# Optimization experiments

Measured on AMD Instinct MI355X. Metric: run time of the kernel, lower is better.

The kernel has to match this reference:

```python
import jax, jax.numpy as jnp
import numpy as np

EMBED_DIM = 768
NUM_HEADS = 12
FF_DIM = 3072
HEAD_DIM = EMBED_DIM // NUM_HEADS
LN_EPS = 1e-5


def setup_inputs() -> dict:
    key = jax.random.key(0)
    ks = jax.random.split(key, 10)
    C, F = EMBED_DIM, FF_DIM
    s = lambda d: 1.0 / np.sqrt(d)
    return {
        "x": jax.random.normal(ks[0], (2, 2048, C), dtype=jnp.float32),
        "w_qkv": jax.random.normal(ks[1], (C, 3 * C), dtype=jnp.float32) * s(C),
        "w_out": jax.random.normal(ks[2], (C, C), dtype=jnp.float32) * s(C),
        "ln1_g": jnp.ones((C,), jnp.float32),
        "ln1_b": jnp.zeros((C,), jnp.float32),
        "ln2_g": jnp.ones((C,), jnp.float32),
        "ln2_b": jnp.zeros((C,), jnp.float32),
        "w1": jax.random.normal(ks[3], (C, F), dtype=jnp.float32) * s(C),
        "b1": jnp.zeros((F,), jnp.float32),
        "w2": jax.random.normal(ks[4], (F, C), dtype=jnp.float32) * s(F),
        "b2": jnp.zeros((C,), jnp.float32),
    }


def _layernorm(x, g, b):
    mu = jnp.mean(x, axis=-1, keepdims=True)
    var = jnp.var(x, axis=-1, keepdims=True)
    return (x - mu) * jax.lax.rsqrt(var + LN_EPS) * g + b


def _attention(x, w_qkv, w_out):
    B, T, C = x.shape
    qkv = x @ w_qkv                               # [B,T,3C]
    q, k, v = jnp.split(qkv, 3, axis=2)
    def heads(t):  # [B,T,C] -> [B,H,T,Dh]
        return t.reshape(B, T, NUM_HEADS, HEAD_DIM).transpose(0, 2, 1, 3)
    q, k, v = heads(q), heads(k), heads(v)
    att = jnp.einsum("bhqd,bhkd->bhqk", q, k) / np.sqrt(HEAD_DIM)
    mask = jnp.tril(jnp.ones((T, T), bool))
    att = jnp.where(mask, att, -jnp.inf)
    att = jax.nn.softmax(att, axis=-1)
    out = jnp.einsum("bhqk,bhkd->bhqd", att, v)   # [B,H,T,Dh]
    out = out.transpose(0, 2, 1, 3).reshape(B, T, C)
    return out @ w_out


def reference(x, w_qkv, w_out, ln1_g, ln1_b, ln2_g, ln2_b, w1, b1, w2, b2):
    x = x + _attention(_layernorm(x, ln1_g, ln1_b), w_qkv, w_out)
    h = _layernorm(x, ln2_g, ln2_b)
    h = jax.nn.gelu(h @ w1 + b1, approximate=False) @ w2 + b2
    return x + h
```

## Files before the change

kernel.cpp:

```cpp
#include <hip/hip_runtime.h>
#include <hip/hip_bf16.h>
#include <math.h>

typedef __attribute__((ext_vector_type(8))) short short8;
typedef __attribute__((ext_vector_type(4))) float f32x4;
typedef __attribute__((address_space(1))) const void CG;
typedef __attribute__((address_space(3))) void LS;

#define LOAD_LDS16(src, dst) __builtin_amdgcn_global_load_lds((CG*)(src), (LS*)(dst), 16, 0, 0)

__device__ __forceinline__ short f2bf(float f) {
  union { float f; unsigned u; } v; v.f = f;
  unsigned r = v.u + 0x7fffu + ((v.u >> 16) & 1u);
  return (short)(r >> 16);
}

__global__ __launch_bounds__(256) void transp_all(const float* __restrict__ w_qkv,
                                                  const float* __restrict__ w_out,
                                                  const float* __restrict__ w1,
                                                  const float* __restrict__ w2,
                                                  short* __restrict__ wqkvT,
                                                  short* __restrict__ woutT,
                                                  short* __restrict__ w1T,
                                                  short* __restrict__ w2T) {
  __shared__ short t[32][33];
  int bid = blockIdx.x;
  const float* W; short* Wt; int K, N, nx, id;
  if (bid < 1728)      { W = w_qkv; Wt = wqkvT; K = 768;  N = 2304; nx = 72; id = bid; }
  else if (bid < 2304) { W = w_out; Wt = woutT; K = 768;  N = 768;  nx = 24; id = bid - 1728; }
  else if (bid < 4608) { W = w1;    Wt = w1T;   K = 768;  N = 3072; nx = 96; id = bid - 2304; }
  else                 { W = w2;    Wt = w2T;   K = 3072; N = 768;  nx = 24; id = bid - 4608; }
  int n0 = (id % nx) << 5, k0 = (id / nx) << 5;
  int tid = threadIdx.x;
#pragma unroll
  for (int p = 0; p < 4; ++p) {
    int e = tid + (p << 8);
    int r = e >> 5, c = e & 31;
    t[r][c] = f2bf(W[(size_t)(k0 + r) * N + n0 + c]);
  }
  __syncthreads();
#pragma unroll
  for (int p = 0; p < 4; ++p) {
    int e = tid + (p << 8);
    int r = e >> 5, c = e & 31;
    Wt[(size_t)(n0 + r) * K + k0 + c] = t[c][r];
  }
}

__global__ __launch_bounds__(256) void ln_kernel(const float* __restrict__ x,
                                                 const float* __restrict__ g,
                                                 const float* __restrict__ b,
                                                 short* __restrict__ out) {
  int row = blockIdx.x;
  const float* xr = x + (size_t)row * 768;
  int tid = threadIdx.x;
  float v0 = xr[tid], v1 = xr[tid + 256], v2 = xr[tid + 512];
  float s = v0 + v1 + v2;
  float ss = v0 * v0 + v1 * v1 + v2 * v2;
#pragma unroll
  for (int m = 1; m < 64; m <<= 1) { s += __shfl_xor(s, m); ss += __shfl_xor(ss, m); }
  __shared__ float red[8];
  int w = tid >> 6;
  if ((tid & 63) == 0) { red[w] = s; red[w + 4] = ss; }
  __syncthreads();
  s = red[0] + red[1] + red[2] + red[3];
  ss = red[4] + red[5] + red[6] + red[7];
  float mean = s * (1.0f / 768.0f);
  float var = ss * (1.0f / 768.0f) - mean * mean;
  float rs = rsqrtf(var + 1e-5f);
  short* outr = out + (size_t)row * 768;
  outr[tid]       = f2bf((v0 - mean) * rs * g[tid]       + b[tid]);
  outr[tid + 256] = f2bf((v1 - mean) * rs * g[tid + 256] + b[tid + 256]);
  outr[tid + 512] = f2bf((v2 - mean) * rs * g[tid + 512] + b[tid + 512]);
}

template <int EPI>
__global__ __launch_bounds__(256, 2) void gemm_bt(
    const short* __restrict__ A, const short* __restrict__ Bt,
    int M, int N, int K,
    short* __restrict__ outQ, short* __restrict__ outK, short* __restrict__ outVt,
    float* __restrict__ outF, short* __restrict__ outB,
    const float* __restrict__ bias, const float* __restrict__ resid) {
  __shared__ short lA[2][128 * 32];
  __shared__ short lB[2][128 * 32];
  int tid = threadIdx.x;
  int lane = tid & 63, w = tid >> 6;
  int li = lane & 15, g = lane >> 4;

  int nx = gridDim.x, ny = gridDim.y;
  int nwg = nx * ny;
  int fid = (int)blockIdx.y * nx + (int)blockIdx.x;
  int nid = (fid & 7) * (nwg >> 3) + (fid >> 3);
  const int GM = 8;
  int npg = GM * nx;
  int grp = nid / npg;
  int fm = grp * GM;
  int gs = min(GM, ny - fm);
  int lid = nid - grp * npg;
  int bm = (fm + lid % gs) << 7;
  int bn = (lid / gs) << 7;

  int wrow = (w >> 1) << 6, wcol = (w & 1) << 6;
  size_t lda = (EPI == 4) ? 3072 : (size_t)K;
  int koff = (EPI == 4) ? (int)blockIdx.z * 1536 : 0;

  const short* as[2];
  const short* bs[2];
#pragma unroll
  for (int p = 0; p < 2; ++p) {
    int v = tid + (p << 8);
    int row = v >> 2;
    int lc = (v & 3) ^ ((row ^ (row >> 2)) & 3);
    as[p] = A + (size_t)(bm + row) * lda + koff + lc * 8;
    bs[p] = Bt + (size_t)(bn + row) * lda + koff + lc * 8;
  }
  int sg = (g ^ ((li ^ (li >> 2)) & 3)) << 3;

  f32x4 zero = {0.f, 0.f, 0.f, 0.f};
  f32x4 acc[4][4];
#pragma unroll
  for (int i = 0; i < 4; ++i)
#pragma unroll
    for (int j = 0; j < 4; ++j) acc[i][j] = zero;

#define GSTAGE(buf, ki)                                                 \
  do {                                                                  \
    int kk = (ki) << 5;                                                 \
    LOAD_LDS16(as[0] + kk, (char*)lA[buf] + (w << 10));                 \
    LOAD_LDS16(as[1] + kk, (char*)lA[buf] + 4096 + (w << 10));          \
    LOAD_LDS16(bs[0] + kk, (char*)lB[buf] + (w << 10));                 \
    LOAD_LDS16(bs[1] + kk, (char*)lB[buf] + 4096 + (w << 10));          \
  } while (0)

  int nk = K >> 5;
  GSTAGE(0, 0);
  for (int ki = 0; ki < nk; ++ki) {
    int cur = ki & 1;
    __syncthreads();
    if (ki + 1 < nk) GSTAGE(cur ^ 1, ki + 1);
    const short* lAc = lA[cur];
    const short* lBc = lB[cur];
    short8 af[4], bf[4];
#pragma unroll
    for (int rt = 0; rt < 4; ++rt)
      af[rt] = *(const short8*)&lAc[(wrow + rt * 16 + li) * 32 + sg];
#pragma unroll
    for (int ct = 0; ct < 4; ++ct)
      bf[ct] = *(const short8*)&lBc[(wcol + ct * 16 + li) * 32 + sg];
#pragma unroll
    for (int rt = 0; rt < 4; ++rt)
#pragma unroll
      for (int ct = 0; ct < 4; ++ct)
        acc[rt][ct] = __builtin_amdgcn_mfma_f32_16x16x32_bf16(af[rt], bf[ct], acc[rt][ct], 0, 0, 0);
  }
#undef GSTAGE

#pragma unroll
  for (int rt = 0; rt < 4; ++rt) {
    int mbase = bm + wrow + rt * 16 + g * 4;
#pragma unroll
    for (int ct = 0; ct < 4; ++ct) {
      int n = bn + wcol + ct * 16 + li;
      f32x4 c = acc[rt][ct];
      if (EPI == 0) {
        if (n < 768) {
          int h = n >> 6, d = n & 63;
#pragma unroll
          for (int i = 0; i < 4; ++i) {
            int tok = mbase + i;
            int bb = tok >> 11, t = tok & 2047;
            outQ[((size_t)((bb * 12 + h) * 2048 + t) << 6) + d] = f2bf(c[i]);
          }
        } else if (n < 1536) {
          int nn = n - 768;
          int h = nn >> 6, d = nn & 63;
#pragma unroll
          for (int i = 0; i < 4; ++i) {
            int tok = mbase + i;
            int bb = tok >> 11, t = tok & 2047;
            outK[((size_t)((bb * 12 + h) * 2048 + t) << 6) + d] = f2bf(c[i]);
          }
        } else {
          int nn = n - 1536;
          int h = nn >> 6, d = nn & 63;
          int bb = mbase >> 11, t = mbase & 2047;
          ushort4 pk;
          pk.x = (unsigned short)f2bf(c[0]);
          pk.y = (unsigned short)f2bf(c[1]);
          pk.z = (unsigned short)f2bf(c[2]);
          pk.w = (unsigned short)f2bf(c[3]);
          *(ushort4*)((unsigned short*)outVt + (((size_t)((bb * 12 + h) * 64 + d)) << 11) + t) = pk;
        }
      } else if (EPI == 1) {
#pragma unroll
        for (int i = 0; i < 4; ++i) {
          int m = mbase + i;
          outF[(size_t)m * N + n] = c[i] + resid[(size_t)m * N + n];
        }
      } else if (EPI == 2) {
        float bv = bias[n];
#pragma unroll
        for (int i = 0; i < 4; ++i) {
          int m = mbase + i;
          float xx = c[i] + bv;
          float gel = 0.5f * xx * (1.0f + erff(xx * 0.70710678118654752f));
          outB[(size_t)m * N + n] = f2bf(gel);
        }
      } else if (EPI == 3) {
        float bv = bias[n];
#pragma unroll
        for (int i = 0; i < 4; ++i) {
          int m = mbase + i;
          outF[(size_t)m * N + n] = c[i] + bv + resid[(size_t)m * N + n];
        }
      } else {
        bool last = (blockIdx.z == 1);
        float bv = last ? bias[n] : 0.f;
#pragma unroll
        for (int i = 0; i < 4; ++i) {
          int m = mbase + i;
          float add = c[i] + bv + (last ? resid[(size_t)m * N + n] : 0.f);
          atomicAdd(&outF[(size_t)m * N + n], add);
        }
      }
    }
  }
}

__global__ __launch_bounds__(256, 3) void attn_kernel(const short* __restrict__ Q,
                                                      const short* __restrict__ Kk,
                                                      const short* __restrict__ Vt,
                                                      unsigned short* __restrict__ o_part,
                                                      float* __restrict__ ml_part) {
  __shared__ short lK[2][64 * 64];
  __shared__ short lV[2][64 * 64];
  __shared__ short lP[4][32 * 64];
  int tid = threadIdx.x;
  int lane = tid & 63, w = tid >> 6;
  int li = lane & 15, g = lane >> 4;
  int bh = blockIdx.y;
  int cid = 39 - (int)blockIdx.x;
  int qt = 0, cum = 0;
  while (true) { int n = (qt >> 2) + 1; if (cid < cum + n) break; cum += n; ++qt; }
  int c = cid - cum;
  int nch = (qt >> 2) + 1;
  int nt = (qt + 1) << 1;
  int bq = nt / nch, rem = nt % nch;
  int t0 = c * bq + (c < rem ? c : rem);
  int t1 = t0 + bq + (c < rem ? 1 : 0);

  int qbase = (qt << 7) + (w << 5);
  const short* Qb = Q + ((size_t)bh << 17);
  const short* Kb = Kk + ((size_t)bh << 17);
  const short* Vb = Vt + ((size_t)bh << 17);

  short8 qf[2][2];
#pragma unroll
  for (int rt = 0; rt < 2; ++rt)
#pragma unroll
    for (int kc = 0; kc < 2; ++kc)
      qf[rt][kc] = *(const short8*)&Qb[(size_t)(qbase + rt * 16 + li) * 64 + kc * 32 + g * 8];

  int r0 = tid >> 3, s0 = (tid & 7) ^ (r0 & 7);
  int r1 = r0 + 32,  s1 = (tid & 7) ^ (r1 & 7);
  const short* kS0 = Kb + r0 * 64 + s0 * 8;
  const short* kS1 = Kb + r1 * 64 + s1 * 8;
  const short* vS0 = Vb + (size_t)r0 * 2048 + s0 * 8;
  const short* vS1 = Vb + (size_t)r1 * 2048 + s1 * 8;

#define STAGE(buf, kt)                                                        \
  do {                                                                        \
    LOAD_LDS16(kS0 + (size_t)(kt) * 4096, (char*)lK[buf] + (w << 10));        \
    LOAD_LDS16(kS1 + (size_t)(kt) * 4096, (char*)lK[buf] + 4096 + (w << 10)); \
    LOAD_LDS16(vS0 + (size_t)(kt) * 64,   (char*)lV[buf] + (w << 10));        \
    LOAD_LDS16(vS1 + (size_t)(kt) * 64,   (char*)lV[buf] + 4096 + (w << 10)); \
  } while (0)

  const short8 kOnes = {0x3F80, 0x3F80, 0x3F80, 0x3F80, 0x3F80, 0x3F80, 0x3F80, 0x3F80};
  f32x4 zero = {0.f, 0.f, 0.f, 0.f};
  f32x4 o[2][4];
  f32x4 lrow[2];
  float mrow[2] = {-1e30f, -1e30f};
#pragma unroll
  for (int rt = 0; rt < 2; ++rt) {
    lrow[rt] = zero;
#pragma unroll
    for (int ct = 0; ct < 4; ++ct) o[rt][ct] = zero;
  }

  int diagKt = qbase >> 6;
  const float SCALE = 0.18033688011112042f;
  int sw = li & 7;
  unsigned short* Pw = (unsigned short*)lP[w];

  STAGE(0, t0);

  for (int kt = t0; kt < t1; ++kt) {
    int cur = (kt - t0) & 1;
    __syncthreads();
    if (kt + 1 < t1) STAGE(cur ^ 1, kt + 1);

    if (kt <= diagKt) {
      const short* Kc = lK[cur];
      const short* Vc = lV[cur];

      f32x4 s[2][4];
#pragma unroll
      for (int rt = 0; rt < 2; ++rt)
#pragma unroll
        for (int ct = 0; ct < 4; ++ct) s[rt][ct] = zero;
#pragma unroll
      for (int kc = 0; kc < 2; ++kc)
#pragma unroll
        for (int ct = 0; ct < 4; ++ct) {
          short8 kf = *(const short8*)&Kc[(ct * 16 + li) * 64 + ((((kc << 2) | g) ^ sw) << 3)];
#pragma unroll
          for (int rt = 0; rt < 2; ++rt)
            s[rt][ct] = __builtin_amdgcn_mfma_f32_16x16x32_bf16(qf[rt][kc], kf, s[rt][ct], 0, 0, 0);
        }

      if (kt == diagKt) {
        int kb0 = kt << 6;
#pragma unroll
        for (int rt = 0; rt < 2; ++rt) {
          int qrow0 = qbase + rt * 16 + g * 4;
#pragma unroll
          for (int ct = 0; ct < 4; ++ct) {
            int kcol = kb0 + ct * 16 + li;
#pragma unroll
            for (int i = 0; i < 4; ++i)
              if (kcol > qrow0 + i) s[rt][ct][i] = -1e30f;
          }
        }
      }

#pragma unroll
      for (int rt = 0; rt < 2; ++rt) {
        float tm = s[rt][0][0];
#pragma unroll
        for (int ct = 0; ct < 4; ++ct)
#pragma unroll
          for (int i = 0; i < 4; ++i) tm = fmaxf(tm, s[rt][ct][i]);
#pragma unroll
        for (int m2 = 1; m2 < 64; m2 <<= 1) tm = fmaxf(tm, __shfl_xor(tm, m2));
        if (tm > mrow[rt] + 8.0f) {
          float corr = exp2f((mrow[rt] - tm) * SCALE);
          mrow[rt] = tm;
#pragma unroll
          for (int i = 0; i < 4; ++i) lrow[rt][i] *= corr;
#pragma unroll
          for (int ct = 0; ct < 4; ++ct)
#pragma unroll
            for (int i = 0; i < 4; ++i) o[rt][ct][i] *= corr;
        }
#pragma unroll
        for (int ct = 0; ct < 4; ++ct)
#pragma unroll
          for (int i = 0; i < 4; ++i) {
            float p = exp2f((s[rt][ct][i] - mrow[rt]) * SCALE);
            int row = rt * 16 + (g << 2) + i;
            int col = (ct << 4) + li;
            int ch = (col >> 3) ^ (row & 7);
            Pw[(row << 6) + (ch << 3) + (col & 7)] = (unsigned short)f2bf(p);
          }
      }

      f32x4 psum[2];
      psum[0] = zero; psum[1] = zero;
#pragma unroll
      for (int kc = 0; kc < 2; ++kc) {
        short8 vf[4];
#pragma unroll
        for (int ct = 0; ct < 4; ++ct)
          vf[ct] = *(const short8*)&Vc[(ct * 16 + li) * 64 + ((((kc << 2) | g) ^ sw) << 3)];
#pragma unroll
        for (int rt = 0; rt < 2; ++rt) {
          short8 pf = *(const short8*)&lP[w][(rt * 16 + li) * 64 + ((((kc << 2) | g) ^ sw) << 3)];
#pragma unroll
          for (int ct = 0; ct < 4; ++ct)
            o[rt][ct] = __builtin_amdgcn_mfma_f32_16x16x32_bf16(pf, vf[ct], o[rt][ct], 0, 0, 0);
          psum[rt] = __builtin_amdgcn_mfma_f32_16x16x32_bf16(pf, kOnes, psum[rt], 0, 0, 0);
        }
      }
#pragma unroll
      for (int rt = 0; rt < 2; ++rt)
#pragma unroll
        for (int i = 0; i < 4; ++i) lrow[rt][i] += psum[rt][i];
    }
  }
#undef STAGE

  int pid = bh * 40 + cid;
#pragma unroll
  for (int rt = 0; rt < 2; ++rt)
#pragma unroll
    for (int ct = 0; ct < 4; ++ct) {
      int col = (ct << 4) + li;
      int row0 = (w << 5) + (rt << 4) + (g << 2);
      ushort4 pk;
      pk.x = (unsigned short)f2bf(o[rt][ct][0]);
      pk.y = (unsigned short)f2bf(o[rt][ct][1]);
      pk.z = (unsigned short)f2bf(o[rt][ct][2]);
      pk.w = (unsigned short)f2bf(o[rt][ct][3]);
      *(ushort4*)&o_part[((size_t)pid * 64 + col) * 128 + row0] = pk;
    }
  if (li == 0) {
    float2* mlp = (float2*)ml_part;
#pragma unroll
    for (int rt = 0; rt < 2; ++rt)
#pragma unroll
      for (int i = 0; i < 4; ++i) {
        int row = (w << 5) + (rt << 4) + (g << 2) + i;
        mlp[(size_t)pid * 128 + row] = make_float2(mrow[rt], lrow[rt][i]);
      }
  }
}

__global__ __launch_bounds__(256) void attn_combine(const unsigned short* __restrict__ o_part,
                                                    const float* __restrict__ ml_part,
                                                    short* __restrict__ O) {
  __shared__ float wgt[4][128];
  int qt = blockIdx.x, bh = blockIdx.y;
  int a = qt >> 2, bb = qt & 3;
  int c0 = 2 * a * (a - 1) + a * bb + qt;
  int nch = a + 1;
  int pid0 = bh * 40 + c0;
  int tid = threadIdx.x;
  const float SCALE = 0.18033688011112042f;
  const float2* mlp = (const float2*)ml_part;

  if (tid < 128) {
    int row = tid;
    float mv[4] = {-1e30f, -1e30f, -1e30f, -1e30f};
    float lv[4] = {0.f, 0.f, 0.f, 0.f};
#pragma unroll
    for (int c = 0; c < 4; ++c)
      if (c < nch) {
        float2 ml = mlp[(size_t)(pid0 + c) * 128 + row];
        mv[c] = ml.x; lv[c] = ml.y;
      }
    float M = fmaxf(fmaxf(mv[0], mv[1]), fmaxf(mv[2], mv[3]));
    float u[4];
    float L = 0.f;
#pragma unroll
    for (int c = 0; c < 4; ++c) {
      u[c] = (c < nch) ? exp2f((mv[c] - M) * SCALE) : 0.f;
      L += lv[c] * u[c];
    }
    float inv = 1.0f / L;
#pragma unroll
    for (int c = 0; c < 4; ++c) wgt[c][row] = u[c] * inv;
  }
  __syncthreads();

  int col = tid & 63, rg = tid >> 6;
  int b = bh / 12, h = bh % 12;
  size_t obase[4];
#pragma unroll
  for (int c = 0; c < 4; ++c) obase[c] = ((size_t)(pid0 + c) * 64 + col) * 128;
  for (int r = 0; r < 32; ++r) {
    int row = (rg << 5) + r;
    float acc = 0.f;
#pragma unroll
    for (int c = 0; c < 4; ++c)
      if (c < nch) {
        union { unsigned u; float f; } cv;
        cv.u = ((unsigned)o_part[obase[c] + row]) << 16;
        acc += cv.f * wgt[c][row];
      }
    int t = (qt << 7) + row;
    O[((size_t)(b * 2048 + t)) * 768 + h * 64 + col] = f2bf(acc);
  }
}

extern "C" void kernel_launch(void* const* d_in, const int* in_sizes, int n_in,
                              void* d_out, int out_size, void* d_ws, size_t ws_size,
                              hipStream_t stream) {
  const float* x     = (const float*)d_in[0];
  const float* w_qkv = (const float*)d_in[1];
  const float* w_out = (const float*)d_in[2];
  const float* ln1g  = (const float*)d_in[3];
  const float* ln1b  = (const float*)d_in[4];
  const float* ln2g  = (const float*)d_in[5];
  const float* ln2b  = (const float*)d_in[6];
  const float* w1    = (const float*)d_in[7];
  const float* b1    = (const float*)d_in[8];
  const float* w2    = (const float*)d_in[9];
  const float* b2    = (const float*)d_in[10];
  float* out = (float*)d_out;
  char* ws = (char*)d_ws;

  short* wqkvT = (short*)(ws + 0);
  short* woutT = (short*)(ws + 3538944);
  short* w1T   = (short*)(ws + 4718592);
  short* w2T   = (short*)(ws + 9437184);
  short* qb    = (short*)(ws + 14155776);
  short* kb    = (short*)(ws + 20447232);
  short* vtb   = (short*)(ws + 26738688);
  short* attnb = (short*)(ws + 33030144);
  short* ab    = qb;
  short* xnb   = (short*)(ws + 39321600);
  float* x2b   = (float*)(ws + 45613056);
  unsigned short* o_part = (unsigned short*)(ws + 39321600);
  float* ml_part = (float*)(ws + 55050240);

  transp_all<<<dim3(6912), 256, 0, stream>>>(w_qkv, w_out, w1, w2, wqkvT, woutT, w1T, w2T);

  ln_kernel<<<dim3(4096), 256, 0, stream>>>(x, ln1g, ln1b, xnb);

  gemm_bt<0><<<dim3(18, 32), 256, 0, stream>>>(xnb, wqkvT, 4096, 2304, 768,
                                               qb, kb, vtb, nullptr, nullptr, nullptr, nullptr);

  attn_kernel<<<dim3(40, 24), 256, 0, stream>>>(qb, kb, vtb, o_part, ml_part);
  attn_combine<<<dim3(16, 24), 256, 0, stream>>>(o_part, ml_part, attnb);

  gemm_bt<1><<<dim3(6, 32), 256, 0, stream>>>(attnb, woutT, 4096, 768, 768,
                                              nullptr, nullptr, nullptr, x2b, nullptr, nullptr, x);

  ln_kernel<<<dim3(4096), 256, 0, stream>>>(x2b, ln2g, ln2b, xnb);

  gemm_bt<2><<<dim3(24, 32), 256, 0, stream>>>(xnb, w1T, 4096, 3072, 768,
                                               nullptr, nullptr, nullptr, nullptr, ab, b1, nullptr);

  hipMemsetAsync(out, 0, (size_t)4096 * 768 * 4, stream);
  gemm_bt<4><<<dim3(6, 32, 2), 256, 0, stream>>>(ab, w2T, 4096, 768, 1536,
                                                 nullptr, nullptr, nullptr, out, nullptr, b2, x2b);
}
```

Before: 243.8 us.

## Widen GEMM tiles to 128x256 with 512-thread workgroups

Replaces the 256-thread 128x128 GEMM with a 512-thread kernel that computes a 128x256 output tile using 8 waves in a 2x4 arrangement, so each A tile loaded into LDS is reused across twice as many columns. Grids are halved along N for all four GEMMs. The aim is to cut global-to-LDS traffic per FLOP. The cost is fewer workgroups, which hurts occupancy and wave balance on small GEMMs such as the 768-wide out-projection (96 blocks) and doubles LDS per block. It also drops the unused EPI==3 epilogue.

Measured after the change: 263.4 us. 1.08x slower.

```diff
diff --git a/kernel.cpp b/kernel.cpp
--- a/kernel.cpp
+++ b/kernel.cpp
@@ -75,17 +75,18 @@
 }
 
 template <int EPI>
-__global__ __launch_bounds__(256, 2) void gemm_bt(
+__global__ __launch_bounds__(512, 4) void gemm512(
     const short* __restrict__ A, const short* __restrict__ Bt,
     int M, int N, int K,
     short* __restrict__ outQ, short* __restrict__ outK, short* __restrict__ outVt,
     float* __restrict__ outF, short* __restrict__ outB,
     const float* __restrict__ bias, const float* __restrict__ resid) {
   __shared__ short lA[2][128 * 32];
-  __shared__ short lB[2][128 * 32];
+  __shared__ short lB[2][256 * 32];
   int tid = threadIdx.x;
   int lane = tid & 63, w = tid >> 6;
   int li = lane & 15, g = lane >> 4;
+  int wr = w >> 2, wc = w & 3;
 
   int nx = gridDim.x, ny = gridDim.y;
   int nwg = nx * ny;
@@ -98,23 +99,24 @@
   int gs = min(GM, ny - fm);
   int lid = nid - grp * npg;
   int bm = (fm + lid % gs) << 7;
-  int bn = (lid / gs) << 7;
-
-  int wrow = (w >> 1) << 6, wcol = (w & 1) << 6;
+  int bn = (lid / gs) << 8;
+
   size_t lda = (EPI == 4) ? 3072 : (size_t)K;
   int koff = (EPI == 4) ? (int)blockIdx.z * 1536 : 0;
 
-  const short* as[2];
-  const short* bs[2];
-#pragma unroll
-  for (int p = 0; p < 2; ++p) {
-    int v = tid + (p << 8);
-    int row = v >> 2;
-    int lc = (v & 3) ^ ((row ^ (row >> 2)) & 3);
-    as[p] = A + (size_t)(bm + row) * lda + koff + lc * 8;
-    bs[p] = Bt + (size_t)(bn + row) * lda + koff + lc * 8;
-  }
-  int sg = (g ^ ((li ^ (li >> 2)) & 3)) << 3;
+  int lr = lane >> 2;
+  int lcs = (lane & 3) ^ ((lr ^ (lr >> 2)) & 3);
+  const short* aSrc  = A + (size_t)(bm + w * 16 + lr) * lda + koff + lcs * 8;
+  const short* bSrc0 = Bt + (size_t)(bn + w * 32 + lr) * lda + koff + lcs * 8;
+  const short* bSrc1 = Bt + (size_t)(bn + w * 32 + 16 + lr) * lda + koff + lcs * 8;
+
+#define STG(buf, ki)                                                  \
+  do {                                                                \
+    int kk = (ki) << 5;                                               \
+    LOAD_LDS16(aSrc + kk, (char*)lA[buf] + (w << 10));                \
+    LOAD_LDS16(bSrc0 + kk, (char*)lB[buf] + (w << 11));               \
+    LOAD_LDS16(bSrc1 + kk, (char*)lB[buf] + (w << 11) + 1024);        \
+  } while (0)
 
   f32x4 zero = {0.f, 0.f, 0.f, 0.f};
   f32x4 acc[4][4];
@@ -123,44 +125,37 @@
 #pragma unroll
     for (int j = 0; j < 4; ++j) acc[i][j] = zero;
 
-#define GSTAGE(buf, ki)                                                 \
-  do {                                                                  \
-    int kk = (ki) << 5;                                                 \
-    LOAD_LDS16(as[0] + kk, (char*)lA[buf] + (w << 10));                 \
-    LOAD_LDS16(as[1] + kk, (char*)lA[buf] + 4096 + (w << 10));          \
-    LOAD_LDS16(bs[0] + kk, (char*)lB[buf] + (w << 10));                 \
-    LOAD_LDS16(bs[1] + kk, (char*)lB[buf] + 4096 + (w << 10));          \
-  } while (0)
+  int sg = (g ^ ((li ^ (li >> 2)) & 3)) << 3;
 
   int nk = K >> 5;
-  GSTAGE(0, 0);
+  STG(0, 0);
   for (int ki = 0; ki < nk; ++ki) {
     int cur = ki & 1;
     __syncthreads();
-    if (ki + 1 < nk) GSTAGE(cur ^ 1, ki + 1);
-    const short* lAc = lA[cur];
-    const short* lBc = lB[cur];
+    if (ki + 1 < nk) STG(cur ^ 1, ki + 1);
+    const short* Ac = lA[cur];
+    const short* Bc = lB[cur];
     short8 af[4], bf[4];
 #pragma unroll
     for (int rt = 0; rt < 4; ++rt)
-      af[rt] = *(const short8*)&lAc[(wrow + rt * 16 + li) * 32 + sg];
+      af[rt] = *(const short8*)&Ac[(wr * 64 + rt * 16 + li) * 32 + sg];
 #pragma unroll
     for (int ct = 0; ct < 4; ++ct)
-      bf[ct] = *(const short8*)&lBc[(wcol + ct * 16 + li) * 32 + sg];
+      bf[ct] = *(const short8*)&Bc[(wc * 64 + ct * 16 + li) * 32 + sg];
 #pragma unroll
     for (int rt = 0; rt < 4; ++rt)
 #pragma unroll
       for (int ct = 0; ct < 4; ++ct)
         acc[rt][ct] = __builtin_amdgcn_mfma_f32_16x16x32_bf16(af[rt], bf[ct], acc[rt][ct], 0, 0, 0);
   }
-#undef GSTAGE
+#undef STG
 
 #pragma unroll
   for (int rt = 0; rt < 4; ++rt) {
-    int mbase = bm + wrow + rt * 16 + g * 4;
+    int mbase = bm + wr * 64 + rt * 16 + g * 4;
 #pragma unroll
     for (int ct = 0; ct < 4; ++ct) {
-      int n = bn + wcol + ct * 16 + li;
+      int n = bn + wc * 64 + ct * 16 + li;
       f32x4 c = acc[rt][ct];
       if (EPI == 0) {
         if (n < 768) {
@@ -205,13 +200,6 @@
           float xx = c[i] + bv;
           float gel = 0.5f * xx * (1.0f + erff(xx * 0.70710678118654752f));
           outB[(size_t)m * N + n] = f2bf(gel);
-        }
-      } else if (EPI == 3) {
-        float bv = bias[n];
-#pragma unroll
-        for (int i = 0; i < 4; ++i) {
-          int m = mbase + i;
-          outF[(size_t)m * N + n] = c[i] + bv + resid[(size_t)m * N + n];
         }
       } else {
         bool last = (blockIdx.z == 1);
@@ -508,21 +496,21 @@
 
   ln_kernel<<<dim3(4096), 256, 0, stream>>>(x, ln1g, ln1b, xnb);
 
-  gemm_bt<0><<<dim3(18, 32), 256, 0, stream>>>(xnb, wqkvT, 4096, 2304, 768,
-                                               qb, kb, vtb, nullptr, nullptr, nullptr, nullptr);
+  gemm512<0><<<dim3(9, 32), 512, 0, stream>>>(xnb, wqkvT, 4096, 2304, 768,
+                                              qb, kb, vtb, nullptr, nullptr, nullptr, nullptr);
 
   attn_kernel<<<dim3(40, 24), 256, 0, stream>>>(qb, kb, vtb, o_part, ml_part);
   attn_combine<<<dim3(16, 24), 256, 0, stream>>>(o_part, ml_part, attnb);
 
-  gemm_bt<1><<<dim3(6, 32), 256, 0, stream>>>(attnb, woutT, 4096, 768, 768,
+  gemm512<1><<<dim3(3, 32), 512, 0, stream>>>(attnb, woutT, 4096, 768, 768,
                                               nullptr, nullptr, nullptr, x2b, nullptr, nullptr, x);
 
   ln_kernel<<<dim3(4096), 256, 0, stream>>>(x2b, ln2g, ln2b, xnb);
 
-  gemm_bt<2><<<dim3(24, 32), 256, 0, stream>>>(xnb, w1T, 4096, 3072, 768,
+  gemm512<2><<<dim3(12, 32), 512, 0, stream>>>(xnb, w1T, 4096, 3072, 768,
                                                nullptr, nullptr, nullptr, nullptr, ab, b1, nullptr);
 
   hipMemsetAsync(out, 0, (size_t)4096 * 768 * 4, stream);
-  gemm_bt<4><<<dim3(6, 32, 2), 256, 0, stream>>>(ab, w2T, 4096, 768, 1536,
+  gemm512<4><<<dim3(3, 32, 2), 512, 0, stream>>>(ab, w2T, 4096, 768, 1536,
                                                  nullptr, nullptr, nullptr, out, nullptr, b2, x2b);
 }
```
